# Kernel tuning notes

Measured on AMD Instinct MI355X. Metric: run time of the kernel, lower is better.

Reference implementation:

```python
import jax, jax.numpy as jnp
import numpy as np

N_NODES = 349525  # complete 4-ary tree, depth 10: (4**10 - 1) / 3
X_SIZE = 128
H_SIZE = 128


def setup_inputs() -> dict:
    key = jax.random.key(0)
    ks = jax.random.split(key, 6)
    s = 0.05  # keep gates out of saturation
    return {
        "x": jax.random.normal(ks[0], (N_NODES, X_SIZE), jnp.float32),
        "W_iou": jax.random.normal(ks[1], (X_SIZE, 3 * H_SIZE), jnp.float32) * s,
        "U_iou": jax.random.normal(ks[2], (H_SIZE, 3 * H_SIZE), jnp.float32) * s,
        "b_iou": jnp.zeros((3 * H_SIZE,), jnp.float32),
        "W_f": jax.random.normal(ks[3], (X_SIZE, H_SIZE), jnp.float32) * s,
        "U_f": jax.random.normal(ks[4], (H_SIZE, H_SIZE), jnp.float32) * s,
        "b_f": jnp.zeros((H_SIZE,), jnp.float32),
        "depth": 10,
        "branching": 4,
    }


def _apply_node(iou, c_sum):
    # apply_node_func: i,o,u gates then cell/hidden update
    i, o, u = jnp.split(iou, 3, axis=-1)
    c = jax.nn.sigmoid(i) * jnp.tanh(u) + c_sum
    h = jax.nn.sigmoid(o) * jnp.tanh(c)
    return h, c


def reference(x, W_iou, U_iou, b_iou, W_f, U_f, b_f, depth, branching):
    # Nodes are in BFS order of a complete `branching`-ary forest-tree;
    # level l occupies [off[l], off[l+1]) and the children of level l are
    # exactly level l+1 (contiguous, `branching` per parent).
    H = b_f.shape[-1]
    off = [(branching ** l - 1) // (branching - 1) for l in range(depth + 1)]

    node_iou = x @ W_iou + b_iou  # [N, 3H]  (W_iou(x) + b_iou)
    node_f = x @ W_f + b_f        # [N, H]   (W_f(x) + b_f)

    h_levels = [None] * depth
    c_levels = [None] * depth

    # Leaves: mailbox empty -> h_tilda = 0, c = 0
    s, e = off[depth - 1], off[depth]
    h, c = _apply_node(node_iou[s:e], jnp.zeros((e - s, H), x.dtype))
    h_levels[depth - 1], c_levels[depth - 1] = h, c

    # Bottom-up topological propagation
    for l in range(depth - 2, -1, -1):
        s, e = off[l], off[l + 1]
        nl = e - s
        ch_h = h_levels[l + 1].reshape(nl, branching, H)  # mailbox['h']
        ch_c = c_levels[l + 1].reshape(nl, branching, H)  # mailbox['c']
        h_tilda = ch_h.sum(axis=1)
        # f = sigmoid(U_f(mailbox.h) + node_f[:, None])
        f = jax.nn.sigmoid(jnp.einsum("nkh,hg->nkg", ch_h, U_f) + node_f[s:e][:, None, :])
        c_sum = (f * ch_c).sum(axis=1)
        iou = node_iou[s:e] + h_tilda @ U_iou
        h, c = _apply_node(iou, c_sum)
        h_levels[l], c_levels[l] = h, c

    h_all = jnp.concatenate(h_levels, axis=0)
    c_all = jnp.concatenate(c_levels, axis=0)
    return h_all, c_all
```

## Files before the change

### kernel.cpp

```cpp
#include <hip/hip_runtime.h>

#define H 128

typedef __bf16 bf16x8 __attribute__((ext_vector_type(8)));
typedef float f32x4 __attribute__((ext_vector_type(4)));

__device__ __forceinline__ float fsig(float x) {
  return __builtin_amdgcn_rcpf(1.0f + __expf(-x));
}
__device__ __forceinline__ float ftanh(float x) {
  float ax = fabsf(x), e = __expf(-2.0f * ax);
  float t = (1.0f - e) * __builtin_amdgcn_rcpf(1.0f + e);
  return x < 0.0f ? -t : t;
}
__device__ __forceinline__ uint2 pack4(float a, float b, float c, float d) {
  union { __bf16 h[4]; uint2 u; } r;
  r.h[0] = (__bf16)a; r.h[1] = (__bf16)b; r.h[2] = (__bf16)c; r.h[3] = (__bf16)d;
  return r.u;
}
__device__ __forceinline__ unsigned swz(unsigned row, unsigned colByte, unsigned rowBytes) {
  return (row * rowBytes + colByte) ^ ((row & 7) << 4);
}

__global__ __launch_bounds__(256)
void prep_weights(const float* __restrict__ W_iou, const float* __restrict__ U_iou,
                  const float* __restrict__ W_f, const float* __restrict__ U_f,
                  uint4* __restrict__ ws)
{
  int item = blockIdx.x * 256 + threadIdx.x;
  float v[8];
  if (item < 2048) {
    int fj = item >> 8, rem = item & 255, ks = rem >> 6, lane = rem & 63;
    int n = fj * 16 + (lane & 15), kb = ks * 32 + (lane >> 4) * 8;
    #pragma unroll
    for (int j = 0; j < 8; j++) v[j] = U_f[(kb + j) * H + n];
  } else if (item < 4096) {
    int i2 = item - 2048;
    int fj = i2 >> 8, rem = i2 & 255, ks = rem >> 6, lane = rem & 63;
    int n = fj * 16 + (lane & 15), kb = ks * 32 + (lane >> 4) * 8;
    #pragma unroll
    for (int j = 0; j < 8; j++) v[j] = W_f[(kb + j) * H + n];
  } else {
    int i2 = item - 4096;
    int fj = i2 >> 9, rem = i2 & 511, ks = rem >> 6, lane = rem & 63;
    int col = (fj >> 3) * 128 + (fj & 7) * 16 + (lane & 15);
    int kb = ks * 32 + (lane >> 4) * 8;
    #pragma unroll
    for (int j = 0; j < 8; j++) {
      int k = kb + j;
      v[j] = (k < 128) ? W_iou[k * 384 + col] : U_iou[(k - 128) * 384 + col];
    }
  }
  union { __bf16 h[8]; uint4 u; } r;
  #pragma unroll
  for (int j = 0; j < 8; j++) r.h[j] = (__bf16)v[j];
  ws[item] = r.u;
}

__global__ __launch_bounds__(256)
void leaf5(const float* __restrict__ x, const __bf16* __restrict__ iou_fmt,
           const float* __restrict__ b_iou,
           float* __restrict__ h_glob, float* __restrict__ c_glob, int leaf_start)
{
  __shared__ __align__(16) char As[64 * 256];
  const int t = threadIdx.x;
  const int m0 = leaf_start + blockIdx.x * 64;

  #pragma unroll
  for (int i = 0; i < 8; i++) {
    int idx = t + i * 256;
    int r = idx >> 5, k0 = (idx & 31) << 2;
    f32x4 v = *reinterpret_cast<const f32x4*>(&x[(size_t)(m0 + r) * H + k0]);
    *reinterpret_cast<uint2*>(As + swz(r, k0 * 2, 256)) = pack4(v.x, v.y, v.z, v.w);
  }
  __syncthreads();

  const int lane = t & 63, w = t >> 6;
  const int l15 = lane & 15, l4 = lane >> 4;

  #pragma unroll 1
  for (int j = 0; j < 2; j++) {
    f32x4 acc[4][3] = {};
    #pragma unroll
    for (int ks = 0; ks < 4; ks++) {
      bf16x8 a[4], b[3];
      #pragma unroll
      for (int m = 0; m < 4; m++)
        a[m] = *reinterpret_cast<const bf16x8*>(As + swz(m * 16 + l15, (ks * 32 + l4 * 8) * 2, 256));
      #pragma unroll
      for (int g = 0; g < 3; g++) {
        int nf = g * 8 + 2 * w + j;
        b[g] = *reinterpret_cast<const bf16x8*>(iou_fmt + ((size_t)(nf * 8 + ks) * 64 + lane) * 8);
      }
      #pragma unroll
      for (int m = 0; m < 4; m++)
        #pragma unroll
        for (int g = 0; g < 3; g++)
          acc[m][g] = __builtin_amdgcn_mfma_f32_16x16x32_bf16(a[m], b[g], acc[m][g], 0, 0, 0);
    }

    int ch = (2 * w + j) * 16 + l15;
    float bi = b_iou[ch], bo = b_iou[H + ch], bu = b_iou[2 * H + ch];
    #pragma unroll
    for (int m = 0; m < 4; m++) {
      int rowb = m * 16 + l4 * 4;
      #pragma unroll
      for (int r = 0; r < 4; r++) {
        size_t o = (size_t)(m0 + rowb + r) * H + ch;
        float c = fsig(acc[m][0][r] + bi) * ftanh(acc[m][2][r] + bu);
        float h = fsig(acc[m][1][r] + bo) * ftanh(c);
        h_glob[o] = h;
        c_glob[o] = c;
      }
    }
  }
}

__global__ __launch_bounds__(256)
void fused_level(const float* __restrict__ x, const __bf16* __restrict__ uf_fmt,
                 const __bf16* __restrict__ wf_fmt, const __bf16* __restrict__ iou_fmt,
                 const float* __restrict__ b_iou, const float* __restrict__ b_f,
                 float* __restrict__ h_glob, float* __restrict__ c_glob,
                 int pstart, int cstart)
{
  __shared__ __align__(16) char CH[128 * 256];
  __shared__ __align__(16) char XH[32 * 512];
  __shared__ float SC[32][128];
  const int t = threadIdx.x;
  const int p0 = blockIdx.x * 32;
  const int c0 = blockIdx.x * 128;

  #pragma unroll
  for (int i = 0; i < 4; i++) {
    int idx = t + i * 256;
    int p = idx >> 5, k0 = (idx & 31) << 2;
    f32x4 s = {};
    #pragma unroll
    for (int j = 0; j < 4; j++) {
      f32x4 v = *reinterpret_cast<const f32x4*>(&h_glob[(size_t)(cstart + c0 + p * 4 + j) * H + k0]);
      *reinterpret_cast<uint2*>(CH + swz(p * 4 + j, k0 * 2, 256)) = pack4(v.x, v.y, v.z, v.w);
      s += v;
    }
    *reinterpret_cast<uint2*>(XH + swz(p, (128 + k0) * 2, 512)) = pack4(s.x, s.y, s.z, s.w);
  }
  #pragma unroll
  for (int i = 0; i < 4; i++) {
    int idx = t + i * 256;
    int p = idx >> 5, k0 = (idx & 31) << 2;
    f32x4 v = *reinterpret_cast<const f32x4*>(&x[(size_t)(pstart + p0 + p) * H + k0]);
    *reinterpret_cast<uint2*>(XH + swz(p, k0 * 2, 512)) = pack4(v.x, v.y, v.z, v.w);
  }
  __syncthreads();

  const int lane = t & 63, w = t >> 6;
  const int l15 = lane & 15, l4 = lane >> 4;

  {
    f32x4 acc[2][2] = {};
    #pragma unroll
    for (int ks = 0; ks < 4; ks++) {
      bf16x8 a[2], b[2];
      #pragma unroll
      for (int m = 0; m < 2; m++)
        a[m] = *reinterpret_cast<const bf16x8*>(XH + swz(m * 16 + l15, (ks * 32 + l4 * 8) * 2, 512));
      #pragma unroll
      for (int n = 0; n < 2; n++) {
        int nf = 2 * w + n;
        b[n] = *reinterpret_cast<const bf16x8*>(wf_fmt + ((size_t)(nf * 4 + ks) * 64 + lane) * 8);
      }
      #pragma unroll
      for (int m = 0; m < 2; m++)
        #pragma unroll
        for (int n = 0; n < 2; n++)
          acc[m][n] = __builtin_amdgcn_mfma_f32_16x16x32_bf16(a[m], b[n], acc[m][n], 0, 0, 0);
    }
    #pragma unroll
    for (int m = 0; m < 2; m++)
      #pragma unroll
      for (int n = 0; n < 2; n++)
        #pragma unroll
        for (int r = 0; r < 4; r++)
          SC[m * 16 + l4 * 4 + r][(2 * w + n) * 16 + l15] = acc[m][n][r];
  }
  __syncthreads();

  {
    f32x4 acc[2][8] = {};
    #pragma unroll
    for (int ks = 0; ks < 4; ks++) {
      bf16x8 a[2], b[8];
      #pragma unroll
      for (int m = 0; m < 2; m++)
        a[m] = *reinterpret_cast<const bf16x8*>(CH + swz(w * 32 + m * 16 + l15, (ks * 32 + l4 * 8) * 2, 256));
      #pragma unroll
      for (int n = 0; n < 8; n++)
        b[n] = *reinterpret_cast<const bf16x8*>(uf_fmt + ((size_t)(n * 4 + ks) * 64 + lane) * 8);
      #pragma unroll
      for (int m = 0; m < 2; m++)
        #pragma unroll
        for (int n = 0; n < 8; n++)
          acc[m][n] = __builtin_amdgcn_mfma_f32_16x16x32_bf16(a[m], b[n], acc[m][n], 0, 0, 0);
    }
    #pragma unroll
    for (int m = 0; m < 2; m++) {
      int rbase = w * 32 + m * 16 + l4 * 4;
      int ploc = rbase >> 2;
      #pragma unroll
      for (int n = 0; n < 8; n++) {
        int ch = n * 16 + l15;
        float sfx = SC[ploc][ch] + b_f[ch];
        float cs = 0.0f;
        #pragma unroll
        for (int r = 0; r < 4; r++) {
          float f = fsig(acc[m][n][r] + sfx);
          cs = fmaf(f, c_glob[(size_t)(cstart + c0 + rbase + r) * H + ch], cs);
        }
        SC[ploc][ch] = cs;
      }
    }
  }
  __syncthreads();

  {
    f32x4 acc[2][3][2] = {};
    #pragma unroll
    for (int ks = 0; ks < 8; ks++) {
      bf16x8 a[2], b[3][2];
      #pragma unroll
      for (int m = 0; m < 2; m++)
        a[m] = *reinterpret_cast<const bf16x8*>(XH + swz(m * 16 + l15, (ks * 32 + l4 * 8) * 2, 512));
      #pragma unroll
      for (int g = 0; g < 3; g++)
        #pragma unroll
        for (int j = 0; j < 2; j++) {
          int nf = g * 8 + 2 * w + j;
          b[g][j] = *reinterpret_cast<const bf16x8*>(iou_fmt + ((size_t)(nf * 8 + ks) * 64 + lane) * 8);
        }
      #pragma unroll
      for (int m = 0; m < 2; m++)
        #pragma unroll
        for (int g = 0; g < 3; g++)
          #pragma unroll
          for (int j = 0; j < 2; j++)
            acc[m][g][j] = __builtin_amdgcn_mfma_f32_16x16x32_bf16(a[m], b[g][j], acc[m][g][j], 0, 0, 0);
    }
    #pragma unroll
    for (int j = 0; j < 2; j++) {
      int ch = (2 * w + j) * 16 + l15;
      float bi = b_iou[ch], bo = b_iou[H + ch], bu = b_iou[2 * H + ch];
      #pragma unroll
      for (int m = 0; m < 2; m++) {
        #pragma unroll
        for (int r = 0; r < 4; r++) {
          int ploc = m * 16 + l4 * 4 + r;
          float gi = acc[m][0][j][r] + bi;
          float go = acc[m][1][j][r] + bo;
          float gu = acc[m][2][j][r] + bu;
          float cs = SC[ploc][ch];
          float c = fsig(gi) * ftanh(gu) + cs;
          float h = fsig(go) * ftanh(c);
          size_t o = (size_t)(pstart + p0 + ploc) * H + ch;
          h_glob[o] = h;
          c_glob[o] = c;
        }
      }
    }
  }
}

#define SNR 4
#define SRP 2
#define BR 4

__global__ __launch_bounds__(256)
void small_kernel(const float* __restrict__ x,
                  const float* __restrict__ W_iou, const float* __restrict__ b_iou,
                  const float* __restrict__ U_iou, const float* __restrict__ W_f,
                  const float* __restrict__ U_f, const float* __restrict__ b_f,
                  float* __restrict__ h_out, float* __restrict__ c_out,
                  int lvl_start, int child_start, int n_lvl)
{
  __shared__ float xs[SNR][H];
  __shared__ float hs[SNR * BR][H];
  __shared__ float ht[SNR][H];
  const int t = threadIdx.x;
  const int node0 = blockIdx.x * SNR;
  const int nrows = min(SNR, n_lvl - node0);

  {
    const f32x4* xgv = reinterpret_cast<const f32x4*>(x + (size_t)(lvl_start + node0) * H);
    f32x4* xsv = reinterpret_cast<f32x4*>(&xs[0][0]);
    int total = nrows * (H / 4);
    for (int i = t; i < total; i += 256) xsv[i] = xgv[i];
  }
  {
    const f32x4* hgv = reinterpret_cast<const f32x4*>(h_out + (size_t)(child_start + node0 * BR) * H);
    f32x4* hsv = reinterpret_cast<f32x4*>(&hs[0][0]);
    int total = nrows * BR * (H / 4);
    for (int i = t; i < total; i += 256) hsv[i] = hgv[i];
  }
  __syncthreads();

  const int ch = t & (H - 1);
  const int g = t >> 7;

  float fx[SRP], ai[SRP], ao[SRP], au[SRP];
  {
    float bi = b_iou[ch], bo = b_iou[ch + H], bu = b_iou[ch + 2 * H], bf = b_f[ch];
    #pragma unroll
    for (int r = 0; r < SRP; r++) { fx[r] = bf; ai[r] = bi; ao[r] = bo; au[r] = bu; }
  }
  {
    const float* wfp = W_f + ch;
    const float* wip = W_iou + ch;
    #pragma unroll 4
    for (int k = 0; k < H; k++) {
      float wf = wfp[k * H];
      float w0 = wip[k * 384], w1 = wip[k * 384 + H], w2 = wip[k * 384 + 2 * H];
      #pragma unroll
      for (int r = 0; r < SRP; r++) {
        float xk = xs[g * SRP + r][k];
        fx[r] = fmaf(xk, wf, fx[r]);
        ai[r] = fmaf(xk, w0, ai[r]);
        ao[r] = fmaf(xk, w1, ao[r]);
        au[r] = fmaf(xk, w2, au[r]);
      }
    }
  }
  #pragma unroll
  for (int r = 0; r < SRP; r++) {
    int row = g * SRP + r;
    float s = hs[row * BR + 0][ch] + hs[row * BR + 1][ch]
            + hs[row * BR + 2][ch] + hs[row * BR + 3][ch];
    ht[row][ch] = s;
  }
  __syncthreads();

  float z[BR][SRP];
  #pragma unroll
  for (int kc = 0; kc < BR; kc++)
    #pragma unroll
    for (int r = 0; r < SRP; r++) z[kc][r] = fx[r];
  {
    const float* ufp = U_f + ch;
    #pragma unroll 4
    for (int m = 0; m < H; m++) {
      float uf = ufp[m * H];
      #pragma unroll
      for (int kc = 0; kc < BR; kc++)
        #pragma unroll
        for (int r = 0; r < SRP; r++)
          z[kc][r] = fmaf(hs[(g * SRP + r) * BR + kc][m], uf, z[kc][r]);
    }
  }
  float csum[SRP];
  #pragma unroll
  for (int r = 0; r < SRP; r++) csum[r] = 0.0f;
  #pragma unroll
  for (int kc = 0; kc < BR; kc++) {
    #pragma unroll
    for (int r = 0; r < SRP; r++) {
      size_t childnode = (size_t)child_start + (size_t)(node0 + g * SRP + r) * BR + kc;
      float f = fsig(z[kc][r]);
      csum[r] = fmaf(f, c_out[childnode * H + ch], csum[r]);
    }
  }
  {
    const float* uip = U_iou + ch;
    #pragma unroll 4
    for (int m = 0; m < H; m++) {
      float w0 = uip[m * 384], w1 = uip[m * 384 + H], w2 = uip[m * 384 + 2 * H];
      #pragma unroll
      for (int r = 0; r < SRP; r++) {
        float hm = ht[g * SRP + r][m];
        ai[r] = fmaf(hm, w0, ai[r]);
        ao[r] = fmaf(hm, w1, ao[r]);
        au[r] = fmaf(hm, w2, au[r]);
      }
    }
  }
  #pragma unroll
  for (int r = 0; r < SRP; r++) {
    int row = g * SRP + r;
    if (row < nrows) {
      float c = fsig(ai[r]) * ftanh(au[r]) + csum[r];
      float h = fsig(ao[r]) * ftanh(c);
      size_t node = (size_t)(lvl_start + node0 + row);
      h_out[node * H + ch] = h;
      c_out[node * H + ch] = c;
    }
  }
}

extern "C" void kernel_launch(void* const* d_in, const int* in_sizes, int n_in,
                              void* d_out, int out_size, void* d_ws, size_t ws_size,
                              hipStream_t stream)
{
  const float* x     = (const float*)d_in[0];
  const float* W_iou = (const float*)d_in[1];
  const float* U_iou = (const float*)d_in[2];
  const float* b_iou = (const float*)d_in[3];
  const float* W_f   = (const float*)d_in[4];
  const float* U_f   = (const float*)d_in[5];
  const float* b_f   = (const float*)d_in[6];
  const int N = 349525;

  float* h_out = (float*)d_out;
  float* c_out = h_out + (size_t)N * H;

  const __bf16* uf_fmt  = (const __bf16*)d_ws;
  const __bf16* wf_fmt  = (const __bf16*)d_ws + 16384;
  const __bf16* iou_fmt = (const __bf16*)d_ws + 32768;

  int off[11];
  off[0] = 0;
  for (int l = 1; l <= 10; l++) off[l] = off[l - 1] * 4 + 1;

  prep_weights<<<64, 256, 0, stream>>>(W_iou, U_iou, W_f, U_f, (uint4*)d_ws);

  leaf5<<<4096, 256, 0, stream>>>(x, iou_fmt, b_iou, h_out, c_out, off[9]);

  for (int l = 8; l >= 4; l--) {
    int n_par = off[l + 1] - off[l];
    fused_level<<<n_par / 32, 256, 0, stream>>>(x, uf_fmt, wf_fmt, iou_fmt, b_iou, b_f,
                                                h_out, c_out, off[l], off[l + 1]);
  }

  for (int l = 3; l >= 0; l--) {
    int s = off[l], e = off[l + 1];
    int n = e - s;
    int grid = (n + SNR - 1) / SNR;
    small_kernel<<<grid, 256, 0, stream>>>(x, W_iou, b_iou, U_iou, W_f, U_f, b_f,
                                           h_out, c_out, s, e, n);
  }
}
```

Before: 399.4 us.

## Fuse leaf and level-8 into one kernel; merge top four levels into single-block kernel

Each level-8 block first computes its own 128 leaf children with the MFMA iou path, then runs the shared fused body to produce its 32 parents. This removes one launch and keeps the children local to the block, though the leaf h/c are still written to and reread from global memory. The four top levels (85 nodes) now run in one single-block kernel that loops over levels with the MFMA fused body, replacing four launches of the FP32 scalar small_kernel. The trade-off is that the top levels run serially in one block, and the leaf work is spread over fewer blocks (2048 instead of 4096), which lowers parallelism.

```diff
diff --git a/kernel.cpp b/kernel.cpp
--- a/kernel.cpp
+++ b/kernel.cpp
@@ -57,63 +57,224 @@
   ws[item] = r.u;
 }
 
-__global__ __launch_bounds__(256)
-void leaf5(const float* __restrict__ x, const __bf16* __restrict__ iou_fmt,
-           const float* __restrict__ b_iou,
-           float* __restrict__ h_glob, float* __restrict__ c_glob, int leaf_start)
-{
-  __shared__ __align__(16) char As[64 * 256];
+__device__ __forceinline__ void fused_body(
+    const float* __restrict__ x, const __bf16* __restrict__ uf_fmt,
+    const __bf16* __restrict__ wf_fmt, const __bf16* __restrict__ iou_fmt,
+    const float* __restrict__ b_iou, const float* __restrict__ b_f,
+    float* __restrict__ h_glob, float* __restrict__ c_glob,
+    int prow0, int crow0, int npar,
+    char* CH, char* XH, float* SC)
+{
   const int t = threadIdx.x;
-  const int m0 = leaf_start + blockIdx.x * 64;
 
   #pragma unroll
-  for (int i = 0; i < 8; i++) {
+  for (int i = 0; i < 4; i++) {
     int idx = t + i * 256;
-    int r = idx >> 5, k0 = (idx & 31) << 2;
-    f32x4 v = *reinterpret_cast<const f32x4*>(&x[(size_t)(m0 + r) * H + k0]);
-    *reinterpret_cast<uint2*>(As + swz(r, k0 * 2, 256)) = pack4(v.x, v.y, v.z, v.w);
+    int p = idx >> 5, k0 = (idx & 31) << 2;
+    f32x4 s = {};
+    #pragma unroll
+    for (int j = 0; j < 4; j++) {
+      f32x4 v = *reinterpret_cast<const f32x4*>(&h_glob[(size_t)(crow0 + p * 4 + j) * H + k0]);
+      *reinterpret_cast<uint2*>(CH + swz(p * 4 + j, k0 * 2, 256)) = pack4(v.x, v.y, v.z, v.w);
+      s += v;
+    }
+    *reinterpret_cast<uint2*>(XH + swz(p, (128 + k0) * 2, 512)) = pack4(s.x, s.y, s.z, s.w);
+  }
+  #pragma unroll
+  for (int i = 0; i < 4; i++) {
+    int idx = t + i * 256;
+    int p = idx >> 5, k0 = (idx & 31) << 2;
+    f32x4 v = *reinterpret_cast<const f32x4*>(&x[(size_t)(prow0 + p) * H + k0]);
+    *reinterpret_cast<uint2*>(XH + swz(p, k0 * 2, 512)) = pack4(v.x, v.y, v.z, v.w);
   }
   __syncthreads();
 
   const int lane = t & 63, w = t >> 6;
   const int l15 = lane & 15, l4 = lane >> 4;
 
+  {
+    f32x4 acc[2][2] = {};
+    #pragma unroll
+    for (int ks = 0; ks < 4; ks++) {
+      bf16x8 a[2], b[2];
+      #pragma unroll
+      for (int m = 0; m < 2; m++)
+        a[m] = *reinterpret_cast<const bf16x8*>(XH + swz(m * 16 + l15, (ks * 32 + l4 * 8) * 2, 512));
+      #pragma unroll
+      for (int n = 0; n < 2; n++) {
+        int nf = 2 * w + n;
+        b[n] = *reinterpret_cast<const bf16x8*>(wf_fmt + ((size_t)(nf * 4 + ks) * 64 + lane) * 8);
+      }
+      #pragma unroll
+      for (int m = 0; m < 2; m++)
+        #pragma unroll
+        for (int n = 0; n < 2; n++)
+          acc[m][n] = __builtin_amdgcn_mfma_f32_16x16x32_bf16(a[m], b[n], acc[m][n], 0, 0, 0);
+    }
+    #pragma unroll
+    for (int m = 0; m < 2; m++)
+      #pragma unroll
+      for (int n = 0; n < 2; n++)
+        #pragma unroll
+        for (int r = 0; r < 4; r++)
+          SC[(m * 16 + l4 * 4 + r) * 128 + (2 * w + n) * 16 + l15] = acc[m][n][r];
+  }
+  __syncthreads();
+
+  {
+    f32x4 acc[2][8] = {};
+    #pragma unroll
+    for (int ks = 0; ks < 4; ks++) {
+      bf16x8 a[2], b[8];
+      #pragma unroll
+      for (int m = 0; m < 2; m++)
+        a[m] = *reinterpret_cast<const bf16x8*>(CH + swz(w * 32 + m * 16 + l15, (ks * 32 + l4 * 8) * 2, 256));
+      #pragma unroll
+      for (int n = 0; n < 8; n++)
+        b[n] = *reinterpret_cast<const bf16x8*>(uf_fmt + ((size_t)(n * 4 + ks) * 64 + lane) * 8);
+      #pragma unroll
+      for (int m = 0; m < 2; m++)
+        #pragma unroll
+        for (int n = 0; n < 8; n++)
+          acc[m][n] = __builtin_amdgcn_mfma_f32_16x16x32_bf16(a[m], b[n], acc[m][n], 0, 0, 0);
+    }
+    #pragma unroll
+    for (int m = 0; m < 2; m++) {
+      int rbase = w * 32 + m * 16 + l4 * 4;
+      int ploc = rbase >> 2;
+      #pragma unroll
+      for (int n = 0; n < 8; n++) {
+        int ch = n * 16 + l15;
+        float sfx = SC[ploc * 128 + ch] + b_f[ch];
+        float cs = 0.0f;
+        #pragma unroll
+        for (int r = 0; r < 4; r++) {
+          float f = fsig(acc[m][n][r] + sfx);
+          cs = fmaf(f, c_glob[(size_t)(crow0 + rbase + r) * H + ch], cs);
+        }
+        SC[ploc * 128 + ch] = cs;
+      }
+    }
+  }
+  __syncthreads();
+
+  {
+    f32x4 acc[2][3][2] = {};
+    #pragma unroll
+    for (int ks = 0; ks < 8; ks++) {
+      bf16x8 a[2], b[3][2];
+      #pragma unroll
+      for (int m = 0; m < 2; m++)
+        a[m] = *reinterpret_cast<const bf16x8*>(XH + swz(m * 16 + l15, (ks * 32 + l4 * 8) * 2, 512));
+      #pragma unroll
+      for (int g = 0; g < 3; g++)
+        #pragma unroll
+        for (int j = 0; j < 2; j++) {
+          int nf = g * 8 + 2 * w + j;
+          b[g][j] = *reinterpret_cast<const bf16x8*>(iou_fmt + ((size_t)(nf * 8 + ks) * 64 + lane) * 8);
+        }
+      #pragma unroll
+      for (int m = 0; m < 2; m++)
+        #pragma unroll
+        for (int g = 0; g < 3; g++)
+          #pragma unroll
+          for (int j = 0; j < 2; j++)
+            acc[m][g][j] = __builtin_amdgcn_mfma_f32_16x16x32_bf16(a[m], b[g][j], acc[m][g][j], 0, 0, 0);
+    }
+    #pragma unroll
+    for (int j = 0; j < 2; j++) {
+      int ch = (2 * w + j) * 16 + l15;
+      float bi = b_iou[ch], bo = b_iou[H + ch], bu = b_iou[2 * H + ch];
+      #pragma unroll
+      for (int m = 0; m < 2; m++) {
+        #pragma unroll
+        for (int r = 0; r < 4; r++) {
+          int ploc = m * 16 + l4 * 4 + r;
+          if (ploc < npar) {
+            float gi = acc[m][0][j][r] + bi;
+            float go = acc[m][1][j][r] + bo;
+            float gu = acc[m][2][j][r] + bu;
+            float cs = SC[ploc * 128 + ch];
+            float c = fsig(gi) * ftanh(gu) + cs;
+            float h = fsig(go) * ftanh(c);
+            size_t o = (size_t)(prow0 + ploc) * H + ch;
+            h_glob[o] = h;
+            c_glob[o] = c;
+          }
+        }
+      }
+    }
+  }
+}
+
+__global__ __launch_bounds__(256)
+void leaf_l8(const float* __restrict__ x, const __bf16* __restrict__ uf_fmt,
+             const __bf16* __restrict__ wf_fmt, const __bf16* __restrict__ iou_fmt,
+             const float* __restrict__ b_iou, const float* __restrict__ b_f,
+             float* __restrict__ h_glob, float* __restrict__ c_glob,
+             int pstart, int cstart)
+{
+  __shared__ __align__(16) char CH[128 * 256];
+  __shared__ __align__(16) char XH[32 * 512];
+  __shared__ float SC[32 * 128];
+  const int t = threadIdx.x;
+  const int p0 = blockIdx.x * 32;
+  const int c0 = blockIdx.x * 128;
+  const int lane = t & 63, w = t >> 6;
+  const int l15 = lane & 15, l4 = lane >> 4;
+
   #pragma unroll 1
-  for (int j = 0; j < 2; j++) {
-    f32x4 acc[4][3] = {};
-    #pragma unroll
-    for (int ks = 0; ks < 4; ks++) {
-      bf16x8 a[4], b[3];
-      #pragma unroll
-      for (int m = 0; m < 4; m++)
-        a[m] = *reinterpret_cast<const bf16x8*>(As + swz(m * 16 + l15, (ks * 32 + l4 * 8) * 2, 256));
-      #pragma unroll
-      for (int g = 0; g < 3; g++) {
-        int nf = g * 8 + 2 * w + j;
-        b[g] = *reinterpret_cast<const bf16x8*>(iou_fmt + ((size_t)(nf * 8 + ks) * 64 + lane) * 8);
-      }
-      #pragma unroll
-      for (int m = 0; m < 4; m++)
-        #pragma unroll
-        for (int g = 0; g < 3; g++)
-          acc[m][g] = __builtin_amdgcn_mfma_f32_16x16x32_bf16(a[m], b[g], acc[m][g], 0, 0, 0);
-    }
-
-    int ch = (2 * w + j) * 16 + l15;
-    float bi = b_iou[ch], bo = b_iou[H + ch], bu = b_iou[2 * H + ch];
-    #pragma unroll
-    for (int m = 0; m < 4; m++) {
-      int rowb = m * 16 + l4 * 4;
-      #pragma unroll
-      for (int r = 0; r < 4; r++) {
-        size_t o = (size_t)(m0 + rowb + r) * H + ch;
-        float c = fsig(acc[m][0][r] + bi) * ftanh(acc[m][2][r] + bu);
-        float h = fsig(acc[m][1][r] + bo) * ftanh(c);
-        h_glob[o] = h;
-        c_glob[o] = c;
-      }
-    }
-  }
+  for (int sub = 0; sub < 2; sub++) {
+    const int r0 = sub * 64;
+    #pragma unroll
+    for (int i = 0; i < 8; i++) {
+      int idx = t + i * 256;
+      int r = idx >> 5, k0 = (idx & 31) << 2;
+      f32x4 v = *reinterpret_cast<const f32x4*>(&x[(size_t)(cstart + c0 + r0 + r) * H + k0]);
+      *reinterpret_cast<uint2*>(CH + swz(r, k0 * 2, 256)) = pack4(v.x, v.y, v.z, v.w);
+    }
+    __syncthreads();
+
+    #pragma unroll 1
+    for (int j = 0; j < 2; j++) {
+      f32x4 acc[4][3] = {};
+      #pragma unroll
+      for (int ks = 0; ks < 4; ks++) {
+        bf16x8 a[4], b[3];
+        #pragma unroll
+        for (int m = 0; m < 4; m++)
+          a[m] = *reinterpret_cast<const bf16x8*>(CH + swz(m * 16 + l15, (ks * 32 + l4 * 8) * 2, 256));
+        #pragma unroll
+        for (int g = 0; g < 3; g++) {
+          int nf = g * 8 + 2 * w + j;
+          b[g] = *reinterpret_cast<const bf16x8*>(iou_fmt + ((size_t)(nf * 8 + ks) * 64 + lane) * 8);
+        }
+        #pragma unroll
+        for (int m = 0; m < 4; m++)
+          #pragma unroll
+          for (int g = 0; g < 3; g++)
+            acc[m][g] = __builtin_amdgcn_mfma_f32_16x16x32_bf16(a[m], b[g], acc[m][g], 0, 0, 0);
+      }
+      int ch = (2 * w + j) * 16 + l15;
+      float bi = b_iou[ch], bo = b_iou[H + ch], bu = b_iou[2 * H + ch];
+      #pragma unroll
+      for (int m = 0; m < 4; m++) {
+        int rowb = m * 16 + l4 * 4;
+        #pragma unroll
+        for (int r = 0; r < 4; r++) {
+          size_t o = (size_t)(cstart + c0 + r0 + rowb + r) * H + ch;
+          float c = fsig(acc[m][0][r] + bi) * ftanh(acc[m][2][r] + bu);
+          float h = fsig(acc[m][1][r] + bo) * ftanh(c);
+          h_glob[o] = h;
+          c_glob[o] = c;
+        }
+      }
+    }
+    __syncthreads();
+  }
+
+  fused_body(x, uf_fmt, wf_fmt, iou_fmt, b_iou, b_f, h_glob, c_glob,
+             pstart + p0, cstart + c0, 32, CH, XH, SC);
 }
 
 __global__ __launch_bounds__(256)
@@ -125,269 +286,32 @@
 {
   __shared__ __align__(16) char CH[128 * 256];
   __shared__ __align__(16) char XH[32 * 512];
-  __shared__ float SC[32][128];
-  const int t = threadIdx.x;
-  const int p0 = blockIdx.x * 32;
-  const int c0 = blockIdx.x * 128;
-
-  #pragma unroll
-  for (int i = 0; i < 4; i++) {
-    int idx = t + i * 256;
-    int p = idx >> 5, k0 = (idx & 31) << 2;
-    f32x4 s = {};
-    #pragma unroll
-    for (int j = 0; j < 4; j++) {
-      f32x4 v = *reinterpret_cast<const f32x4*>(&h_glob[(size_t)(cstart + c0 + p * 4 + j) * H + k0]);
-      *reinterpret_cast<uint2*>(CH + swz(p * 4 + j, k0 * 2, 256)) = pack4(v.x, v.y, v.z, v.w);
-      s += v;
-    }
-    *reinterpret_cast<uint2*>(XH + swz(p, (128 + k0) * 2, 512)) = pack4(s.x, s.y, s.z, s.w);
-  }
-  #pragma unroll
-  for (int i = 0; i < 4; i++) {
-    int idx = t + i * 256;
-    int p = idx >> 5, k0 = (idx & 31) << 2;
-    f32x4 v = *reinterpret_cast<const f32x4*>(&x[(size_t)(pstart + p0 + p) * H + k0]);
-    *reinterpret_cast<uint2*>(XH + swz(p, k0 * 2, 512)) = pack4(v.x, v.y, v.z, v.w);
-  }
-  __syncthreads();
-
-  const int lane = t & 63, w = t >> 6;
-  const int l15 = lane & 15, l4 = lane >> 4;
-
-  {
-    f32x4 acc[2][2] = {};
-    #pragma unroll
-    for (int ks = 0; ks < 4; ks++) {
-      bf16x8 a[2], b[2];
-      #pragma unroll
-      for (int m = 0; m < 2; m++)
-        a[m] = *reinterpret_cast<const bf16x8*>(XH + swz(m * 16 + l15, (ks * 32 + l4 * 8) * 2, 512));
-      #pragma unroll
-      for (int n = 0; n < 2; n++) {
-        int nf = 2 * w + n;
-        b[n] = *reinterpret_cast<const bf16x8*>(wf_fmt + ((size_t)(nf * 4 + ks) * 64 + lane) * 8);
-      }
-      #pragma unroll
-      for (int m = 0; m < 2; m++)
-        #pragma unroll
-        for (int n = 0; n < 2; n++)
-          acc[m][n] = __builtin_amdgcn_mfma_f32_16x16x32_bf16(a[m], b[n], acc[m][n], 0, 0, 0);
-    }
-    #pragma unroll
-    for (int m = 0; m < 2; m++)
-      #pragma unroll
-      for (int n = 0; n < 2; n++)
-        #pragma unroll
-        for (int r = 0; r < 4; r++)
-          SC[m * 16 + l4 * 4 + r][(2 * w + n) * 16 + l15] = acc[m][n][r];
-  }
-  __syncthreads();
-
-  {
-    f32x4 acc[2][8] = {};
-    #pragma unroll
-    for (int ks = 0; ks < 4; ks++) {
-      bf16x8 a[2], b[8];
-      #pragma unroll
-      for (int m = 0; m < 2; m++)
-        a[m] = *reinterpret_cast<const bf16x8*>(CH + swz(w * 32 + m * 16 + l15, (ks * 32 + l4 * 8) * 2, 256));
-      #pragma unroll
-      for (int n = 0; n < 8; n++)
-        b[n] = *reinterpret_cast<const bf16x8*>(uf_fmt + ((size_t)(n * 4 + ks) * 64 + lane) * 8);
-      #pragma unroll
-      for (int m = 0; m < 2; m++)
-        #pragma unroll
-        for (int n = 0; n < 8; n++)
-          acc[m][n] = __builtin_amdgcn_mfma_f32_16x16x32_bf16(a[m], b[n], acc[m][n], 0, 0, 0);
-    }
-    #pragma unroll
-    for (int m = 0; m < 2; m++) {
-      int rbase = w * 32 + m * 16 + l4 * 4;
-      int ploc = rbase >> 2;
-      #pragma unroll
-      for (int n = 0; n < 8; n++) {
-        int ch = n * 16 + l15;
-        float sfx = SC[ploc][ch] + b_f[ch];
-        float cs = 0.0f;
-        #pragma unroll
-        for (int r = 0; r < 4; r++) {
-          float f = fsig(acc[m][n][r] + sfx);
-          cs = fmaf(f, c_glob[(size_t)(cstart + c0 + rbase + r) * H + ch], cs);
-        }
-        SC[ploc][ch] = cs;
-      }
-    }
-  }
-  __syncthreads();
-
-  {
-    f32x4 acc[2][3][2] = {};
-    #pragma unroll
-    for (int ks = 0; ks < 8; ks++) {
-      bf16x8 a[2], b[3][2];
-      #pragma unroll
-      for (int m = 0; m < 2; m++)
-        a[m] = *reinterpret_cast<const bf16x8*>(XH + swz(m * 16 + l15, (ks * 32 + l4 * 8) * 2, 512));
-      #pragma unroll
-      for (int g = 0; g < 3; g++)
-        #pragma unroll
-        for (int j = 0; j < 2; j++) {
-          int nf = g * 8 + 2 * w + j;
-          b[g][j] = *reinterpret_cast<const bf16x8*>(iou_fmt + ((size_t)(nf * 8 + ks) * 64 + lane) * 8);
-        }
-      #pragma unroll
-      for (int m = 0; m < 2; m++)
-        #pragma unroll
-        for (int g = 0; g < 3; g++)
-          #pragma unroll
-          for (int j = 0; j < 2; j++)
-            acc[m][g][j] = __builtin_amdgcn_mfma_f32_16x16x32_bf16(a[m], b[g][j], acc[m][g][j], 0, 0, 0);
-    }
-    #pragma unroll
-    for (int j = 0; j < 2; j++) {
-      int ch = (2 * w + j) * 16 + l15;
-      float bi = b_iou[ch], bo = b_iou[H + ch], bu = b_iou[2 * H + ch];
-      #pragma unroll
-      for (int m = 0; m < 2; m++) {
-        #pragma unroll
-        for (int r = 0; r < 4; r++) {
-          int ploc = m * 16 + l4 * 4 + r;
-          float gi = acc[m][0][j][r] + bi;
-          float go = acc[m][1][j][r] + bo;
-          float gu = acc[m][2][j][r] + bu;
-          float cs = SC[ploc][ch];
-          float c = fsig(gi) * ftanh(gu) + cs;
-          float h = fsig(go) * ftanh(c);
-          size_t o = (size_t)(pstart + p0 + ploc) * H + ch;
-          h_glob[o] = h;
-          c_glob[o] = c;
-        }
-      }
-    }
-  }
-}
-
-#define SNR 4
-#define SRP 2
-#define BR 4
+  __shared__ float SC[32 * 128];
+  fused_body(x, uf_fmt, wf_fmt, iou_fmt, b_iou, b_f, h_glob, c_glob,
+             pstart + blockIdx.x * 32, cstart + blockIdx.x * 128, 32, CH, XH, SC);
+}
 
 __global__ __launch_bounds__(256)
-void small_kernel(const float* __restrict__ x,
-                  const float* __restrict__ W_iou, const float* __restrict__ b_iou,
-                  const float* __restrict__ U_iou, const float* __restrict__ W_f,
-                  const float* __restrict__ U_f, const float* __restrict__ b_f,
-                  float* __restrict__ h_out, float* __restrict__ c_out,
-                  int lvl_start, int child_start, int n_lvl)
-{
-  __shared__ float xs[SNR][H];
-  __shared__ float hs[SNR * BR][H];
-  __shared__ float ht[SNR][H];
-  const int t = threadIdx.x;
-  const int node0 = blockIdx.x * SNR;
-  const int nrows = min(SNR, n_lvl - node0);
-
-  {
-    const f32x4* xgv = reinterpret_cast<const f32x4*>(x + (size_t)(lvl_start + node0) * H);
-    f32x4* xsv = reinterpret_cast<f32x4*>(&xs[0][0]);
-    int total = nrows * (H / 4);
-    for (int i = t; i < total; i += 256) xsv[i] = xgv[i];
-  }
-  {
-    const f32x4* hgv = reinterpret_cast<const f32x4*>(h_out + (size_t)(child_start + node0 * BR) * H);
-    f32x4* hsv = reinterpret_cast<f32x4*>(&hs[0][0]);
-    int total = nrows * BR * (H / 4);
-    for (int i = t; i < total; i += 256) hsv[i] = hgv[i];
-  }
-  __syncthreads();
-
-  const int ch = t & (H - 1);
-  const int g = t >> 7;
-
-  float fx[SRP], ai[SRP], ao[SRP], au[SRP];
-  {
-    float bi = b_iou[ch], bo = b_iou[ch + H], bu = b_iou[ch + 2 * H], bf = b_f[ch];
-    #pragma unroll
-    for (int r = 0; r < SRP; r++) { fx[r] = bf; ai[r] = bi; ao[r] = bo; au[r] = bu; }
-  }
-  {
-    const float* wfp = W_f + ch;
-    const float* wip = W_iou + ch;
-    #pragma unroll 4
-    for (int k = 0; k < H; k++) {
-      float wf = wfp[k * H];
-      float w0 = wip[k * 384], w1 = wip[k * 384 + H], w2 = wip[k * 384 + 2 * H];
-      #pragma unroll
-      for (int r = 0; r < SRP; r++) {
-        float xk = xs[g * SRP + r][k];
-        fx[r] = fmaf(xk, wf, fx[r]);
-        ai[r] = fmaf(xk, w0, ai[r]);
-        ao[r] = fmaf(xk, w1, ao[r]);
-        au[r] = fmaf(xk, w2, au[r]);
-      }
-    }
-  }
-  #pragma unroll
-  for (int r = 0; r < SRP; r++) {
-    int row = g * SRP + r;
-    float s = hs[row * BR + 0][ch] + hs[row * BR + 1][ch]
-            + hs[row * BR + 2][ch] + hs[row * BR + 3][ch];
-    ht[row][ch] = s;
-  }
-  __syncthreads();
-
-  float z[BR][SRP];
-  #pragma unroll
-  for (int kc = 0; kc < BR; kc++)
-    #pragma unroll
-    for (int r = 0; r < SRP; r++) z[kc][r] = fx[r];
-  {
-    const float* ufp = U_f + ch;
-    #pragma unroll 4
-    for (int m = 0; m < H; m++) {
-      float uf = ufp[m * H];
-      #pragma unroll
-      for (int kc = 0; kc < BR; kc++)
-        #pragma unroll
-        for (int r = 0; r < SRP; r++)
-          z[kc][r] = fmaf(hs[(g * SRP + r) * BR + kc][m], uf, z[kc][r]);
-    }
-  }
-  float csum[SRP];
-  #pragma unroll
-  for (int r = 0; r < SRP; r++) csum[r] = 0.0f;
-  #pragma unroll
-  for (int kc = 0; kc < BR; kc++) {
-    #pragma unroll
-    for (int r = 0; r < SRP; r++) {
-      size_t childnode = (size_t)child_start + (size_t)(node0 + g * SRP + r) * BR + kc;
-      float f = fsig(z[kc][r]);
-      csum[r] = fmaf(f, c_out[childnode * H + ch], csum[r]);
-    }
-  }
-  {
-    const float* uip = U_iou + ch;
-    #pragma unroll 4
-    for (int m = 0; m < H; m++) {
-      float w0 = uip[m * 384], w1 = uip[m * 384 + H], w2 = uip[m * 384 + 2 * H];
-      #pragma unroll
-      for (int r = 0; r < SRP; r++) {
-        float hm = ht[g * SRP + r][m];
-        ai[r] = fmaf(hm, w0, ai[r]);
-        ao[r] = fmaf(hm, w1, ao[r]);
-        au[r] = fmaf(hm, w2, au[r]);
-      }
-    }
-  }
-  #pragma unroll
-  for (int r = 0; r < SRP; r++) {
-    int row = g * SRP + r;
-    if (row < nrows) {
-      float c = fsig(ai[r]) * ftanh(au[r]) + csum[r];
-      float h = fsig(ao[r]) * ftanh(c);
-      size_t node = (size_t)(lvl_start + node0 + row);
-      h_out[node * H + ch] = h;
-      c_out[node * H + ch] = c;
+void top_kernel(const float* __restrict__ x, const __bf16* __restrict__ uf_fmt,
+                const __bf16* __restrict__ wf_fmt, const __bf16* __restrict__ iou_fmt,
+                const float* __restrict__ b_iou, const float* __restrict__ b_f,
+                float* __restrict__ h_glob, float* __restrict__ c_glob)
+{
+  __shared__ __align__(16) char CH[128 * 256];
+  __shared__ __align__(16) char XH[32 * 512];
+  __shared__ float SC[32 * 128];
+  const int ps[4] = {21, 5, 1, 0};
+  const int cs[4] = {85, 21, 5, 1};
+  const int np[4] = {64, 16, 4, 1};
+  #pragma unroll 1
+  for (int li = 0; li < 4; li++) {
+    int ntile = (np[li] + 31) >> 5;
+    #pragma unroll 1
+    for (int tile = 0; tile < ntile; tile++) {
+      int npar = np[li] - tile * 32; if (npar > 32) npar = 32;
+      fused_body(x, uf_fmt, wf_fmt, iou_fmt, b_iou, b_f, h_glob, c_glob,
+                 ps[li] + tile * 32, cs[li] + tile * 128, npar, CH, XH, SC);
+      __syncthreads();
     }
   }
 }
@@ -418,19 +342,14 @@
 
   prep_weights<<<64, 256, 0, stream>>>(W_iou, U_iou, W_f, U_f, (uint4*)d_ws);
 
-  leaf5<<<4096, 256, 0, stream>>>(x, iou_fmt, b_iou, h_out, c_out, off[9]);
-
-  for (int l = 8; l >= 4; l--) {
+  leaf_l8<<<2048, 256, 0, stream>>>(x, uf_fmt, wf_fmt, iou_fmt, b_iou, b_f,
+                                    h_out, c_out, off[8], off[9]);
+
+  for (int l = 7; l >= 4; l--) {
     int n_par = off[l + 1] - off[l];
     fused_level<<<n_par / 32, 256, 0, stream>>>(x, uf_fmt, wf_fmt, iou_fmt, b_iou, b_f,
                                                 h_out, c_out, off[l], off[l + 1]);
   }
 
-  for (int l = 3; l >= 0; l--) {
-    int s = off[l], e = off[l + 1];
-    int n = e - s;
-    int grid = (n + SNR - 1) / SNR;
-    small_kernel<<<grid, 256, 0, stream>>>(x, W_iou, b_iou, U_iou, W_f, U_f, b_f,
-                                           h_out, c_out, s, e, n);
-  }
-}
+  top_kernel<<<1, 256, 0, stream>>>(x, uf_fmt, wf_fmt, iou_fmt, b_iou, b_f, h_out, c_out);
+}
```

Result: slower. 499.6 us (+25.1%).
